# Kernel optimization log

Measured on AMD Instinct MI355X. Metric: run time of the kernel, lower is better.

Reference implementation:

```python
import jax, jax.numpy as jnp
import numpy as np

N, E, B = 100000, 1600000, 64
IN, HID, OUT, ED = 64, 128, 128, 2
K, ALPHA = 16, 0.1
LN_EPS = 1e-5


def setup_inputs() -> dict:
    key = jax.random.key(0)
    ks = jax.random.split(key, 24)
    def gl(k, shape, fan_in):
        return jax.random.uniform(k, shape, jnp.float32, -1.0, 1.0) / np.sqrt(fan_in)
    inp = {
        "x": jax.random.normal(ks[0], (N, IN), jnp.float32),
        "edge_index": jax.random.randint(ks[1], (2, E), 0, N, jnp.int64),
        "batch": jnp.sort(jax.random.randint(ks[2], (N,), 0, B, jnp.int64)),
        "edge_attr": jax.random.normal(ks[3], (E, ED), jnp.float32),
        # conv1: edge lin (ED->IN) + mlp (IN->HID->HID)
        "We1": gl(ks[4], (ED, IN), ED), "be1": jnp.zeros((IN,)),
        "W1a": gl(ks[5], (IN, HID), IN), "b1a": jnp.zeros((HID,)),
        "W1b": gl(ks[6], (HID, HID), HID), "b1b": jnp.zeros((HID,)),
        "g1": jnp.ones((HID,)), "bn1": jnp.zeros((HID,)),
        # conv2: edge lin (ED->HID) + mlp (HID->OUT->OUT)
        "We2": gl(ks[7], (ED, HID), ED), "be2": jnp.zeros((HID,)),
        "W2a": gl(ks[8], (HID, OUT), HID), "b2a": jnp.zeros((OUT,)),
        "W2b": gl(ks[9], (OUT, OUT), OUT), "b2b": jnp.zeros((OUT,)),
        "g2": jnp.ones((OUT,)), "bn2": jnp.zeros((OUT,)),
        # gate nn (OUT -> OUT//2 -> 1)
        "Wg1": gl(ks[10], (OUT, OUT // 2), OUT), "bg1": jnp.zeros((OUT // 2,)),
        "Wg2": gl(ks[11], (OUT // 2, 1), OUT // 2), "bg2": jnp.zeros((1,)),
    }
    return inp


def _gelu(x):
    return jax.nn.gelu(x, approximate=False)


def _layernorm(x, g, b):
    mu = jnp.mean(x, axis=-1, keepdims=True)
    var = jnp.mean(jnp.square(x - mu), axis=-1, keepdims=True)
    return (x - mu) * jax.lax.rsqrt(var + LN_EPS) * g + b


def _gine(x, src, dst, edge_attr, We, be, W1, b1, W2, b2):
    # message: ReLU(x_j + lin(edge_attr)), aggregated by sum at dst; eps=0
    m = jax.nn.relu(x[src] + edge_attr @ We + be)          # [E, d]
    agg = jax.ops.segment_sum(m, dst, num_segments=N)      # [N, d]
    h = x + agg
    return _gelu(h @ W1 + b1) @ W2 + b2


def _appnp(x, src, dst):
    # gcn_norm with self-loops: deg_i = 1 + in-degree
    deg = jax.ops.segment_sum(jnp.ones((E,), x.dtype), dst, num_segments=N) + 1.0
    dis = jax.lax.rsqrt(deg)
    w = dis[src] * dis[dst]            # [E]
    selfw = 1.0 / deg                  # [N]
    def step(i, h):
        prop = jax.ops.segment_sum(w[:, None] * h[src], dst, num_segments=N) \
               + selfw[:, None] * h
        return (1.0 - ALPHA) * prop + ALPHA * x
    return jax.lax.fori_loop(0, K, step, x)


def reference(x, edge_index, batch, edge_attr,
              We1, be1, W1a, b1a, W1b, b1b, g1, bn1,
              We2, be2, W2a, b2a, W2b, b2b, g2, bn2,
              Wg1, bg1, Wg2, bg2):
    src, dst = edge_index[0], edge_index[1]
    h = _gine(x, src, dst, edge_attr, We1, be1, W1a, b1a, W1b, b1b)
    h = _layernorm(_gelu(h), g1, bn1)
    # dropout is identity in eval
    h = _gine(h, src, dst, edge_attr, We2, be2, W2a, b2a, W2b, b2b)
    h = _layernorm(h, g2, bn2)
    h = _appnp(h, src, dst)
    # attentional aggregation: per-graph softmax over gate scores
    gate = (_gelu(h @ Wg1 + bg1) @ Wg2 + bg2)[:, 0]        # [N]
    m = jax.ops.segment_max(gate, batch, num_segments=B)    # [B]
    e = jnp.exp(gate - m[batch])
    s = jax.ops.segment_sum(e, batch, num_segments=B)
    a = e / s[batch]
    g = jax.ops.segment_sum(a[:, None] * h, batch, num_segments=B)  # [B, OUT]
    return h, g
```

## Files before the change

### kernel.cpp

```cpp
#include <hip/hip_runtime.h>
#include <math.h>

#define N_NODES 100000
#define N_EDGES 1600000
#define N_B 64
#define D_IN 64
#define D_HID 128
#define D_OUT 128
#define K_ITER 16
#define LN_EPS 1e-5f

typedef short s8v __attribute__((ext_vector_type(8)));
typedef float f4v __attribute__((ext_vector_type(4)));

__device__ __forceinline__ float gelu_f(float x) {
    return 0.5f * x * (1.0f + erff(0.70710678118654752440f * x));
}

__device__ __forceinline__ float ubx(unsigned u) { return __uint_as_float(u << 16); }
__device__ __forceinline__ float uby(unsigned u) { return __uint_as_float(u & 0xffff0000u); }

__device__ __forceinline__ unsigned short bf_rne(float x) {
    unsigned u = __float_as_uint(x);
    u += 0x7fffu + ((u >> 16) & 1u);
    return (unsigned short)(u >> 16);
}
__device__ __forceinline__ float bf_f(unsigned short s) {
    return __uint_as_float(((unsigned)s) << 16);
}
__device__ __forceinline__ unsigned pack_bf2(float a, float b) {
    return (unsigned)bf_rne(a) | (((unsigned)bf_rne(b)) << 16);
}


__global__ __launch_bounds__(256) void hist_kernel(const int* __restrict__ dst, int* __restrict__ counts) {
    int e = blockIdx.x * 256 + threadIdx.x;
    if (e < N_EDGES) atomicAdd(&counts[dst[e]], 1);
}

__global__ __launch_bounds__(256) void deg_kernel(const int* __restrict__ counts,
                                                  float* __restrict__ dis, float* __restrict__ selfw) {
    int i = blockIdx.x * 256 + threadIdx.x;
    if (i < N_NODES) {
        float d = (float)(counts[i] + 1);
        dis[i] = 1.0f / sqrtf(d);
        selfw[i] = 1.0f / d;
    }
}

__global__ __launch_bounds__(1024) void scan1(const int* __restrict__ counts, int* __restrict__ rp,
                                              int* __restrict__ bsum) {
    __shared__ int tmp[1024];
    int t = threadIdx.x;
    int idx = blockIdx.x * 1024 + t;
    int v = (idx < N_NODES) ? counts[idx] : 0;
    tmp[t] = v;
    __syncthreads();
    for (int o = 1; o < 1024; o <<= 1) {
        int add = (t >= o) ? tmp[t - o] : 0;
        __syncthreads();
        tmp[t] += add;
        __syncthreads();
    }
    if (idx < N_NODES) rp[idx] = tmp[t] - v;
    if (t == 1023) bsum[blockIdx.x] = tmp[t];
}

__global__ void scan2(int* bsum, int nb) {
    if (threadIdx.x == 0 && blockIdx.x == 0) {
        int acc = 0;
        for (int i = 0; i < nb; i++) { int v = bsum[i]; bsum[i] = acc; acc += v; }
    }
}

__global__ __launch_bounds__(1024) void scan3(int* __restrict__ rp, const int* __restrict__ bsum,
                                              int* __restrict__ cursor) {
    int t = threadIdx.x;
    int idx = blockIdx.x * 1024 + t;
    if (idx < N_NODES) {
        int v = rp[idx] + bsum[blockIdx.x];
        rp[idx] = v;
        cursor[idx] = v;
    }
    if (idx == 0) rp[N_NODES] = N_EDGES;
}

__global__ __launch_bounds__(256) void scatter_kernel(const int* __restrict__ src, const int* __restrict__ dst,
                                                      const float* __restrict__ ea,
                                                      int* __restrict__ cursor, int4* __restrict__ edata) {
    int e = blockIdx.x * 256 + threadIdx.x;
    if (e >= N_EDGES) return;
    int s = src[e], d = dst[e];
    int pos = atomicAdd(&cursor[d], 1);
    float2 e2 = ((const float2*)ea)[e];
    int4 v;
    v.x = s;
    v.y = __float_as_int(e2.x);
    v.z = __float_as_int(e2.y);
    v.w = 0;
    edata[pos] = v;
}

__global__ __launch_bounds__(256) void split_kernel(const int4* __restrict__ edata, int* __restrict__ esrc) {
    int e = blockIdx.x * 256 + threadIdx.x;
    if (e < N_EDGES) esrc[e] = edata[e].x;
}


__global__ __launch_bounds__(256) void conv1_gather(const float* __restrict__ x, const int* __restrict__ rp,
                                                    const int4* __restrict__ edata,
                                                    const float* __restrict__ We1, const float* __restrict__ be1,
                                                    float* __restrict__ out) {
    int gw = (blockIdx.x * 256 + threadIdx.x) >> 6;
    if (gw >= N_NODES) return;
    int lane = threadIdx.x & 63;
    float w0 = We1[lane], w1 = We1[64 + lane], bb = be1[lane];
    float acc = x[(size_t)gw * 64 + lane];
    int j = rp[gw], jend = rp[gw + 1];
    for (; j + 8 <= jend; j += 8) {
        int4 e0 = edata[j], e1 = edata[j + 1], e2 = edata[j + 2], e3 = edata[j + 3];
        int4 e4 = edata[j + 4], e5 = edata[j + 5], e6 = edata[j + 6], e7 = edata[j + 7];
        float v0 = x[(size_t)e0.x * 64 + lane];
        float v1 = x[(size_t)e1.x * 64 + lane];
        float v2 = x[(size_t)e2.x * 64 + lane];
        float v3 = x[(size_t)e3.x * 64 + lane];
        float v4 = x[(size_t)e4.x * 64 + lane];
        float v5 = x[(size_t)e5.x * 64 + lane];
        float v6 = x[(size_t)e6.x * 64 + lane];
        float v7 = x[(size_t)e7.x * 64 + lane];
        acc += fmaxf(v0 + __int_as_float(e0.y) * w0 + __int_as_float(e0.z) * w1 + bb, 0.0f);
        acc += fmaxf(v1 + __int_as_float(e1.y) * w0 + __int_as_float(e1.z) * w1 + bb, 0.0f);
        acc += fmaxf(v2 + __int_as_float(e2.y) * w0 + __int_as_float(e2.z) * w1 + bb, 0.0f);
        acc += fmaxf(v3 + __int_as_float(e3.y) * w0 + __int_as_float(e3.z) * w1 + bb, 0.0f);
        acc += fmaxf(v4 + __int_as_float(e4.y) * w0 + __int_as_float(e4.z) * w1 + bb, 0.0f);
        acc += fmaxf(v5 + __int_as_float(e5.y) * w0 + __int_as_float(e5.z) * w1 + bb, 0.0f);
        acc += fmaxf(v6 + __int_as_float(e6.y) * w0 + __int_as_float(e6.z) * w1 + bb, 0.0f);
        acc += fmaxf(v7 + __int_as_float(e7.y) * w0 + __int_as_float(e7.z) * w1 + bb, 0.0f);
    }
    for (; j < jend; j++) {
        int4 e = edata[j];
        float v = x[(size_t)e.x * 64 + lane];
        acc += fmaxf(v + __int_as_float(e.y) * w0 + __int_as_float(e.z) * w1 + bb, 0.0f);
    }
    out[(size_t)gw * 64 + lane] = acc;
}

__global__ __launch_bounds__(256) void conv2_gather(const float* __restrict__ h1f, const unsigned* __restrict__ h1b,
                                                    const int* __restrict__ rp,
                                                    const int4* __restrict__ edata,
                                                    const float* __restrict__ We2, const float* __restrict__ be2,
                                                    float* __restrict__ out) {
    int gw = (blockIdx.x * 256 + threadIdx.x) >> 6;
    if (gw >= N_NODES) return;
    int lane = threadIdx.x & 63;
    int f0 = lane * 2;
    float w00 = We2[f0], w01 = We2[f0 + 1];
    float w10 = We2[128 + f0], w11 = We2[128 + f0 + 1];
    float b0 = be2[f0], b1 = be2[f0 + 1];
    float2 hc = ((const float2*)h1f)[(size_t)gw * 64 + lane];
    float a0 = hc.x, a1 = hc.y;
    int j = rp[gw], jend = rp[gw + 1];
    for (; j + 8 <= jend; j += 8) {
        int4 e0 = edata[j], e1 = edata[j + 1], e2 = edata[j + 2], e3 = edata[j + 3];
        int4 e4 = edata[j + 4], e5 = edata[j + 5], e6 = edata[j + 6], e7 = edata[j + 7];
        unsigned v0 = h1b[(size_t)e0.x * 64 + lane];
        unsigned v1 = h1b[(size_t)e1.x * 64 + lane];
        unsigned v2 = h1b[(size_t)e2.x * 64 + lane];
        unsigned v3 = h1b[(size_t)e3.x * 64 + lane];
        unsigned v4 = h1b[(size_t)e4.x * 64 + lane];
        unsigned v5 = h1b[(size_t)e5.x * 64 + lane];
        unsigned v6 = h1b[(size_t)e6.x * 64 + lane];
        unsigned v7 = h1b[(size_t)e7.x * 64 + lane];
        a0 += fmaxf(ubx(v0) + __int_as_float(e0.y) * w00 + __int_as_float(e0.z) * w10 + b0, 0.0f);
        a1 += fmaxf(uby(v0) + __int_as_float(e0.y) * w01 + __int_as_float(e0.z) * w11 + b1, 0.0f);
        a0 += fmaxf(ubx(v1) + __int_as_float(e1.y) * w00 + __int_as_float(e1.z) * w10 + b0, 0.0f);
        a1 += fmaxf(uby(v1) + __int_as_float(e1.y) * w01 + __int_as_float(e1.z) * w11 + b1, 0.0f);
        a0 += fmaxf(ubx(v2) + __int_as_float(e2.y) * w00 + __int_as_float(e2.z) * w10 + b0, 0.0f);
        a1 += fmaxf(uby(v2) + __int_as_float(e2.y) * w01 + __int_as_float(e2.z) * w11 + b1, 0.0f);
        a0 += fmaxf(ubx(v3) + __int_as_float(e3.y) * w00 + __int_as_float(e3.z) * w10 + b0, 0.0f);
        a1 += fmaxf(uby(v3) + __int_as_float(e3.y) * w01 + __int_as_float(e3.z) * w11 + b1, 0.0f);
        a0 += fmaxf(ubx(v4) + __int_as_float(e4.y) * w00 + __int_as_float(e4.z) * w10 + b0, 0.0f);
        a1 += fmaxf(uby(v4) + __int_as_float(e4.y) * w01 + __int_as_float(e4.z) * w11 + b1, 0.0f);
        a0 += fmaxf(ubx(v5) + __int_as_float(e5.y) * w00 + __int_as_float(e5.z) * w10 + b0, 0.0f);
        a1 += fmaxf(uby(v5) + __int_as_float(e5.y) * w01 + __int_as_float(e5.z) * w11 + b1, 0.0f);
        a0 += fmaxf(ubx(v6) + __int_as_float(e6.y) * w00 + __int_as_float(e6.z) * w10 + b0, 0.0f);
        a1 += fmaxf(uby(v6) + __int_as_float(e6.y) * w01 + __int_as_float(e6.z) * w11 + b1, 0.0f);
        a0 += fmaxf(ubx(v7) + __int_as_float(e7.y) * w00 + __int_as_float(e7.z) * w10 + b0, 0.0f);
        a1 += fmaxf(uby(v7) + __int_as_float(e7.y) * w01 + __int_as_float(e7.z) * w11 + b1, 0.0f);
    }
    for (; j < jend; j++) {
        int4 e = edata[j];
        unsigned v = h1b[(size_t)e.x * 64 + lane];
        a0 += fmaxf(ubx(v) + __int_as_float(e.y) * w00 + __int_as_float(e.z) * w10 + b0, 0.0f);
        a1 += fmaxf(uby(v) + __int_as_float(e.y) * w01 + __int_as_float(e.z) * w11 + b1, 0.0f);
    }
    out[(size_t)gw * 128 + f0] = a0;
    out[(size_t)gw * 128 + f0 + 1] = a1;
}


template <int Kd, bool GELU, bool LN, int OMODE>
__global__ __launch_bounds__(256) void mlp_mfma(const float* __restrict__ A, const float* __restrict__ W,
                                                const float* __restrict__ bias, const float* __restrict__ g,
                                                const float* __restrict__ bn, float* __restrict__ outf,
                                                unsigned short* __restrict__ outb) {
    __shared__ unsigned short sHi[8192];
    __shared__ unsigned short sLo[8192];
    int wave = threadIdx.x >> 6, lane = threadIdx.x & 63;
    int quad = lane >> 4, n = lane & 15;
    int rowA = blockIdx.x * 64 + wave * 16 + n;
    int rowAc = (rowA < N_NODES) ? rowA : 0;

    f4v acc[8];
    #pragma unroll
    for (int t = 0; t < 8; t++) acc[t] = (f4v){0.f, 0.f, 0.f, 0.f};

    for (int ph = 0; ph < Kd / 64; ph++) {
        __syncthreads();
        for (int idx = threadIdx.x; idx < 8192; idx += 256) {
            int k = idx >> 7, c = idx & 127;
            float v = W[(size_t)(ph * 64 + k) * 128 + c];
            unsigned short hi = bf_rne(v);
            unsigned short lo = bf_rne(v - bf_f(hi));
            int kk = k >> 5, q = (k >> 3) & 3, j = k & 7, t = c >> 4, nn = c & 15;
            int lidx = ((((kk * 4 + q) * 8 + t) * 16 + nn) << 3) + j;
            sHi[lidx] = hi;
            sLo[lidx] = lo;
        }
        __syncthreads();
        #pragma unroll
        for (int kk = 0; kk < 2; kk++) {
            int k0 = ph * 64 + kk * 32 + quad * 8;
            const float4* ap = (const float4*)(A + (size_t)rowAc * Kd + k0);
            float4 a0 = ap[0], a1 = ap[1];
            float av[8] = {a0.x, a0.y, a0.z, a0.w, a1.x, a1.y, a1.z, a1.w};
            s8v ahi, alo;
            #pragma unroll
            for (int j = 0; j < 8; j++) {
                unsigned short h = bf_rne(av[j]);
                ahi[j] = (short)h;
                alo[j] = (short)bf_rne(av[j] - bf_f(h));
            }
            int base = ((kk * 4 + quad) * 8) * 128;
            #pragma unroll
            for (int t = 0; t < 8; t++) {
                s8v bhi = *(const s8v*)&sHi[base + ((t * 16 + n) << 3)];
                s8v blo = *(const s8v*)&sLo[base + ((t * 16 + n) << 3)];
                acc[t] = __builtin_amdgcn_mfma_f32_16x16x32_bf16(ahi, bhi, acc[t], 0, 0, 0);
                acc[t] = __builtin_amdgcn_mfma_f32_16x16x32_bf16(ahi, blo, acc[t], 0, 0, 0);
                acc[t] = __builtin_amdgcn_mfma_f32_16x16x32_bf16(alo, bhi, acc[t], 0, 0, 0);
            }
        }
    }

    float bcol[8], gcol[8], bncol[8];
    #pragma unroll
    for (int t = 0; t < 8; t++) {
        bcol[t] = bias[t * 16 + n];
        if (LN) { gcol[t] = g[t * 16 + n]; bncol[t] = bn[t * 16 + n]; }
    }
    #pragma unroll
    for (int r = 0; r < 4; r++) {
        int row = blockIdx.x * 64 + wave * 16 + quad * 4 + r;
        float v[8];
        #pragma unroll
        for (int t = 0; t < 8; t++) {
            float x = acc[t][r] + bcol[t];
            v[t] = GELU ? gelu_f(x) : x;
        }
        if (LN) {
            float s = 0.f, q2 = 0.f;
            #pragma unroll
            for (int t = 0; t < 8; t++) { s += v[t]; q2 += v[t] * v[t]; }
            #pragma unroll
            for (int m = 1; m <= 8; m <<= 1) {
                s += __shfl_xor(s, m, 64);
                q2 += __shfl_xor(q2, m, 64);
            }
            float mu = s * (1.0f / 128.0f);
            float rs = rsqrtf(q2 * (1.0f / 128.0f) - mu * mu + LN_EPS);
            #pragma unroll
            for (int t = 0; t < 8; t++) v[t] = (v[t] - mu) * rs * gcol[t] + bncol[t];
        }
        if (row < N_NODES) {
            #pragma unroll
            for (int t = 0; t < 8; t++) {
                if (OMODE != 2) outf[(size_t)row * 128 + t * 16 + n] = v[t];
                if (OMODE >= 1) outb[(size_t)row * 128 + t * 16 + n] = bf_rne(v[t]);
            }
        }
    }
}


__global__ __launch_bounds__(256) void gate_mfma(const float* __restrict__ h, const float* __restrict__ Wg1,
                                                 const float* __restrict__ bg1, const float* __restrict__ Wg2,
                                                 const float* __restrict__ bg2, float* __restrict__ gate) {
    __shared__ unsigned short sHi[8192];
    __shared__ unsigned short sLo[8192];
    int wave = threadIdx.x >> 6, lane = threadIdx.x & 63;
    int quad = lane >> 4, n = lane & 15;
    for (int idx = threadIdx.x; idx < 8192; idx += 256) {
        int k = idx >> 6, c = idx & 63;
        float v = Wg1[k * 64 + c];
        unsigned short hi = bf_rne(v);
        unsigned short lo = bf_rne(v - bf_f(hi));
        int kk = k >> 5, q = (k >> 3) & 3, j = k & 7, t = c >> 4, nn = c & 15;
        int lidx = ((((kk * 4 + q) * 4 + t) * 16 + nn) << 3) + j;
        sHi[lidx] = hi;
        sLo[lidx] = lo;
    }
    __syncthreads();
    int rowA = blockIdx.x * 64 + wave * 16 + n;
    int rowAc = (rowA < N_NODES) ? rowA : 0;
    f4v acc[4];
    #pragma unroll
    for (int t = 0; t < 4; t++) acc[t] = (f4v){0.f, 0.f, 0.f, 0.f};
    #pragma unroll
    for (int kk = 0; kk < 4; kk++) {
        const float4* ap = (const float4*)(h + (size_t)rowAc * 128 + kk * 32 + quad * 8);
        float4 a0 = ap[0], a1 = ap[1];
        float av[8] = {a0.x, a0.y, a0.z, a0.w, a1.x, a1.y, a1.z, a1.w};
        s8v ahi, alo;
        #pragma unroll
        for (int j = 0; j < 8; j++) {
            unsigned short hh = bf_rne(av[j]);
            ahi[j] = (short)hh;
            alo[j] = (short)bf_rne(av[j] - bf_f(hh));
        }
        int base = ((kk * 4 + quad) * 4) * 128;
        #pragma unroll
        for (int t = 0; t < 4; t++) {
            s8v bhi = *(const s8v*)&sHi[base + ((t * 16 + n) << 3)];
            s8v blo = *(const s8v*)&sLo[base + ((t * 16 + n) << 3)];
            acc[t] = __builtin_amdgcn_mfma_f32_16x16x32_bf16(ahi, bhi, acc[t], 0, 0, 0);
            acc[t] = __builtin_amdgcn_mfma_f32_16x16x32_bf16(ahi, blo, acc[t], 0, 0, 0);
            acc[t] = __builtin_amdgcn_mfma_f32_16x16x32_bf16(alo, bhi, acc[t], 0, 0, 0);
        }
    }
    float b2 = bg2[0];
    float bb[4], vv[4];
    #pragma unroll
    for (int t = 0; t < 4; t++) { bb[t] = bg1[t * 16 + n]; vv[t] = Wg2[t * 16 + n]; }
    #pragma unroll
    for (int r = 0; r < 4; r++) {
        int row = blockIdx.x * 64 + wave * 16 + quad * 4 + r;
        float val = 0.f;
        #pragma unroll
        for (int t = 0; t < 4; t++) val += gelu_f(acc[t][r] + bb[t]) * vv[t];
        #pragma unroll
        for (int m = 1; m <= 8; m <<= 1) val += __shfl_xor(val, m, 64);
        if (n == 0 && row < N_NODES) gate[row] = val + b2;
    }
}


template <bool LAST>
__global__ __launch_bounds__(256) void appnp_step_bf(const unsigned* __restrict__ hin,
                                                     const unsigned* __restrict__ anchor,
                                                     unsigned* __restrict__ hout, float2* __restrict__ houtf,
                                                     const int* __restrict__ rp, const int* __restrict__ esrc,
                                                     const float* __restrict__ dis,
                                                     const float* __restrict__ selfw) {
    int gw = (blockIdx.x * 256 + threadIdx.x) >> 6;
    if (gw >= N_NODES) return;
    int lane = threadIdx.x & 63;
    size_t idx = (size_t)gw * 64 + lane;
    float swi = selfw[gw];
    float wd = dis[gw];
    unsigned hcp = hin[idx];
    float ax = swi * ubx(hcp), ay = swi * uby(hcp);
    int j = rp[gw], jend = rp[gw + 1];
    for (; j + 8 <= jend; j += 8) {
        int s0 = esrc[j],     s1 = esrc[j + 1], s2 = esrc[j + 2], s3 = esrc[j + 3];
        int s4 = esrc[j + 4], s5 = esrc[j + 5], s6 = esrc[j + 6], s7 = esrc[j + 7];
        unsigned v0 = hin[(size_t)s0 * 64 + lane];
        unsigned v1 = hin[(size_t)s1 * 64 + lane];
        unsigned v2 = hin[(size_t)s2 * 64 + lane];
        unsigned v3 = hin[(size_t)s3 * 64 + lane];
        unsigned v4 = hin[(size_t)s4 * 64 + lane];
        unsigned v5 = hin[(size_t)s5 * 64 + lane];
        unsigned v6 = hin[(size_t)s6 * 64 + lane];
        unsigned v7 = hin[(size_t)s7 * 64 + lane];
        float w0 = dis[s0] * wd, w1 = dis[s1] * wd, w2 = dis[s2] * wd, w3 = dis[s3] * wd;
        float w4 = dis[s4] * wd, w5 = dis[s5] * wd, w6 = dis[s6] * wd, w7 = dis[s7] * wd;
        ax = fmaf(w0, ubx(v0), ax); ay = fmaf(w0, uby(v0), ay);
        ax = fmaf(w1, ubx(v1), ax); ay = fmaf(w1, uby(v1), ay);
        ax = fmaf(w2, ubx(v2), ax); ay = fmaf(w2, uby(v2), ay);
        ax = fmaf(w3, ubx(v3), ax); ay = fmaf(w3, uby(v3), ay);
        ax = fmaf(w4, ubx(v4), ax); ay = fmaf(w4, uby(v4), ay);
        ax = fmaf(w5, ubx(v5), ax); ay = fmaf(w5, uby(v5), ay);
        ax = fmaf(w6, ubx(v6), ax); ay = fmaf(w6, uby(v6), ay);
        ax = fmaf(w7, ubx(v7), ax); ay = fmaf(w7, uby(v7), ay);
    }
    for (; j + 4 <= jend; j += 4) {
        int s0 = esrc[j], s1 = esrc[j + 1], s2 = esrc[j + 2], s3 = esrc[j + 3];
        unsigned v0 = hin[(size_t)s0 * 64 + lane];
        unsigned v1 = hin[(size_t)s1 * 64 + lane];
        unsigned v2 = hin[(size_t)s2 * 64 + lane];
        unsigned v3 = hin[(size_t)s3 * 64 + lane];
        float w0 = dis[s0] * wd, w1 = dis[s1] * wd, w2 = dis[s2] * wd, w3 = dis[s3] * wd;
        ax = fmaf(w0, ubx(v0), ax); ay = fmaf(w0, uby(v0), ay);
        ax = fmaf(w1, ubx(v1), ax); ay = fmaf(w1, uby(v1), ay);
        ax = fmaf(w2, ubx(v2), ax); ay = fmaf(w2, uby(v2), ay);
        ax = fmaf(w3, ubx(v3), ax); ay = fmaf(w3, uby(v3), ay);
    }
    for (; j < jend; j++) {
        int s = esrc[j];
        unsigned v = hin[(size_t)s * 64 + lane];
        float w = dis[s] * wd;
        ax = fmaf(w, ubx(v), ax); ay = fmaf(w, uby(v), ay);
    }
    unsigned ancp = anchor[idx];
    float ox = 0.9f * ax + 0.1f * ubx(ancp);
    float oy = 0.9f * ay + 0.1f * uby(ancp);
    if (LAST) {
        float2 o; o.x = ox; o.y = oy;
        houtf[idx] = o;
    } else {
        hout[idx] = pack_bf2(ox, oy);
    }
}


__global__ void seg_begin(const int* __restrict__ batch, int* __restrict__ gbeg) {
    int b = threadIdx.x;
    if (b > N_B) return;
    if (b == N_B) { gbeg[N_B] = N_NODES; return; }
    int lo = 0, hi = N_NODES;
    while (lo < hi) {
        int mid = (lo + hi) >> 1;
        if (batch[mid] < b) lo = mid + 1; else hi = mid;
    }
    gbeg[b] = lo;
}

__global__ __launch_bounds__(256) void seg_max(const float* __restrict__ gate, const int* __restrict__ gbeg,
                                               float* __restrict__ gmax) {
    int b = blockIdx.x;
    int s = gbeg[b], e = gbeg[b + 1];
    float m = -INFINITY;
    for (int i = s + threadIdx.x; i < e; i += 256) m = fmaxf(m, gate[i]);
    for (int o = 32; o > 0; o >>= 1) m = fmaxf(m, __shfl_xor(m, o, 64));
    __shared__ float red[4];
    if ((threadIdx.x & 63) == 0) red[threadIdx.x >> 6] = m;
    __syncthreads();
    if (threadIdx.x == 0) gmax[b] = fmaxf(fmaxf(red[0], red[1]), fmaxf(red[2], red[3]));
}

__global__ __launch_bounds__(256) void seg_sum(const float* __restrict__ gate, const int* __restrict__ gbeg,
                                               const float* __restrict__ gmax, float* __restrict__ gsum) {
    int b = blockIdx.x;
    int s = gbeg[b], e = gbeg[b + 1];
    float m = gmax[b];
    float acc = 0.0f;
    for (int i = s + threadIdx.x; i < e; i += 256) acc += expf(gate[i] - m);
    for (int o = 32; o > 0; o >>= 1) acc += __shfl_xor(acc, o, 64);
    __shared__ float red[4];
    if ((threadIdx.x & 63) == 0) red[threadIdx.x >> 6] = acc;
    __syncthreads();
    if (threadIdx.x == 0) gsum[b] = red[0] + red[1] + red[2] + red[3];
}

__global__ __launch_bounds__(512) void seg_pool(const float* __restrict__ h, const float* __restrict__ gate,
                                                const int* __restrict__ gbeg, const float* __restrict__ gmax,
                                                const float* __restrict__ gsum, float* __restrict__ gout) {
    int b = blockIdx.x >> 3, slice = blockIdx.x & 7;
    int team = threadIdx.x >> 7;
    int f = threadIdx.x & 127;
    int s = gbeg[b], e = gbeg[b + 1];
    float m = gmax[b];
    float inv = (e > s) ? 1.0f / gsum[b] : 0.0f;
    float acc = 0.0f;
    for (int i = s + slice * 4 + team; i < e; i += 32) {
        float a = expf(gate[i] - m) * inv;
        acc = fmaf(a, h[(size_t)i * 128 + f], acc);
    }
    __shared__ float red[4][128];
    red[team][f] = acc;
    __syncthreads();
    if (team == 0) {
        float v = red[0][f] + red[1][f] + red[2][f] + red[3][f];
        atomicAdd(&gout[b * 128 + f], v);
    }
}


extern "C" void kernel_launch(void* const* d_in, const int* in_sizes, int n_in,
                              void* d_out, int out_size, void* d_ws, size_t ws_size,
                              hipStream_t stream) {
    const float* x     = (const float*)d_in[0];
    const int*   ei    = (const int*)d_in[1];
    const int*   batch = (const int*)d_in[2];
    const float* ea    = (const float*)d_in[3];
    const float* We1 = (const float*)d_in[4];
    const float* be1 = (const float*)d_in[5];
    const float* W1a = (const float*)d_in[6];
    const float* b1a = (const float*)d_in[7];
    const float* W1b = (const float*)d_in[8];
    const float* b1b = (const float*)d_in[9];
    const float* g1  = (const float*)d_in[10];
    const float* bn1 = (const float*)d_in[11];
    const float* We2 = (const float*)d_in[12];
    const float* be2 = (const float*)d_in[13];
    const float* W2a = (const float*)d_in[14];
    const float* b2a = (const float*)d_in[15];
    const float* W2b = (const float*)d_in[16];
    const float* b2b = (const float*)d_in[17];
    const float* g2  = (const float*)d_in[18];
    const float* bn2 = (const float*)d_in[19];
    const float* Wg1 = (const float*)d_in[20];
    const float* bg1 = (const float*)d_in[21];
    const float* Wg2 = (const float*)d_in[22];
    const float* bg2 = (const float*)d_in[23];

    float* outH = (float*)d_out;
    float* outG = outH + (size_t)N_NODES * 128;

    char* w = (char*)d_ws;
    auto carve = [&](size_t bytes) {
        void* p = (void*)w;
        w += ((bytes + 255) / 256) * 256;
        return p;
    };
    float*  bufB   = (float*)carve((size_t)N_NODES * 128 * 4);
    float*  bufC   = (float*)carve((size_t)N_NODES * 128 * 4);
    int4*   edata  = (int4*)carve((size_t)N_EDGES * 16);
    int*    counts = (int*)carve((size_t)N_NODES * 4);
    int*    rp     = (int*)carve((size_t)(N_NODES + 1) * 4);
    int*    cursor = (int*)carve((size_t)N_NODES * 4);
    float*  dis    = (float*)carve((size_t)N_NODES * 4);
    float*  selfw  = (float*)carve((size_t)N_NODES * 4);
    float*  gate   = (float*)carve((size_t)N_NODES * 4);
    int*    bsum   = (int*)carve(128 * 4);
    float*  gmax   = (float*)carve(N_B * 4);
    float*  gsum   = (float*)carve(N_B * 4);
    int*    gbeg   = (int*)carve((N_B + 1) * 4);

    const int* src = ei;
    const int* dst = ei + N_EDGES;

    const int NB_SCAN = (N_NODES + 1023) / 1024;
    const int EB = (N_EDGES + 255) / 256;
    const int NBLK = (N_NODES + 255) / 256;
    const int WBLK = (N_NODES + 3) / 4;
    const int MBLK = (N_NODES + 63) / 64;

    hipMemsetAsync(counts, 0, (size_t)N_NODES * 4, stream);
    hist_kernel<<<EB, 256, 0, stream>>>(dst, counts);
    deg_kernel<<<NBLK, 256, 0, stream>>>(counts, dis, selfw);
    scan1<<<NB_SCAN, 1024, 0, stream>>>(counts, rp, bsum);
    scan2<<<1, 64, 0, stream>>>(bsum, NB_SCAN);
    scan3<<<NB_SCAN, 1024, 0, stream>>>(rp, bsum, cursor);
    scatter_kernel<<<EB, 256, 0, stream>>>(src, dst, ea, cursor, edata);

    unsigned short* h1bf  = (unsigned short*)bufC;
    unsigned* ancU  = (unsigned*)bufC;
    unsigned* pingA = ancU + (size_t)N_NODES * 64;
    unsigned* pingB = (unsigned*)bufB;
    int*      esrc  = (int*)(bufB + (size_t)N_NODES * 64);

    conv1_gather<<<WBLK, 256, 0, stream>>>(x, rp, edata, We1, be1, bufB);
    mlp_mfma<64, true, false, 0><<<MBLK, 256, 0, stream>>>(bufB, W1a, b1a, nullptr, nullptr, outH, nullptr);
    mlp_mfma<128, true, true, 1><<<MBLK, 256, 0, stream>>>(outH, W1b, b1b, g1, bn1, bufB, h1bf);

    conv2_gather<<<WBLK, 256, 0, stream>>>(bufB, (const unsigned*)h1bf, rp, edata, We2, be2, outH);
    mlp_mfma<128, true, false, 0><<<MBLK, 256, 0, stream>>>(outH, W2a, b2a, nullptr, nullptr, bufB, nullptr);
    mlp_mfma<128, false, true, 2><<<MBLK, 256, 0, stream>>>(bufB, W2b, b2b, g2, bn2, nullptr, (unsigned short*)ancU);

    split_kernel<<<EB, 256, 0, stream>>>(edata, esrc);

    const unsigned* cur = ancU;
    for (int k = 1; k <= K_ITER - 1; k++) {
        unsigned* dstbuf = (k & 1) ? pingA : pingB;
        appnp_step_bf<false><<<WBLK, 256, 0, stream>>>(cur, ancU, dstbuf, nullptr, rp, esrc, dis, selfw);
        cur = dstbuf;
    }
    appnp_step_bf<true><<<WBLK, 256, 0, stream>>>(cur, ancU, nullptr, (float2*)outH, rp, esrc, dis, selfw);

    gate_mfma<<<MBLK, 256, 0, stream>>>(outH, Wg1, bg1, Wg2, bg2, gate);
    seg_begin<<<1, 128, 0, stream>>>(batch, gbeg);
    seg_max<<<N_B, 256, 0, stream>>>(gate, gbeg, gmax);
    seg_sum<<<N_B, 256, 0, stream>>>(gate, gbeg, gmax, gsum);
    hipMemsetAsync(outG, 0, (size_t)N_B * 128 * 4, stream);
    seg_pool<<<N_B * 8, 512, 0, stream>>>(outH, gate, gbeg, gmax, gsum, outG);
}
```

Measured before the change: 1.860 ms.

## Rescale APPNP state by D^-1/2 to drop per-edge weights; gather conv1 x in bf16

The APPNP iteration now works on u = D^-1/2 h, so each edge contribution is a plain sum and the per-edge dis[src] loads and multiplies are removed. The self-loop and final scale use 0.9*selfw and sqrt(deg). The anchor is pre-scaled by dis when written from the last MLP, and the final step rescales by sqrt(deg) to recover h. Separately, x is converted to bf16 so the conv1 neighbor gather reads half the bytes, at the cost of an extra conversion kernel and reduced precision in the conv1 messages.

New measurement: 1.779 ms. 1.05x faster.

```diff
diff --git a/kernel.cpp b/kernel.cpp
--- a/kernel.cpp
+++ b/kernel.cpp
@@ -39,12 +39,14 @@
 }
 
 __global__ __launch_bounds__(256) void deg_kernel(const int* __restrict__ counts,
-                                                  float* __restrict__ dis, float* __restrict__ selfw) {
+                                                  float* __restrict__ dis, float* __restrict__ selfw,
+                                                  float* __restrict__ rsq) {
     int i = blockIdx.x * 256 + threadIdx.x;
     if (i < N_NODES) {
         float d = (float)(counts[i] + 1);
         dis[i] = 1.0f / sqrtf(d);
         selfw[i] = 1.0f / d;
+        rsq[i] = sqrtf(d);
     }
 }
 
@@ -106,8 +108,21 @@
     if (e < N_EDGES) esrc[e] = edata[e].x;
 }
 
-
-__global__ __launch_bounds__(256) void conv1_gather(const float* __restrict__ x, const int* __restrict__ rp,
+__global__ __launch_bounds__(256) void x_to_bf(const float4* __restrict__ x4, uint2* __restrict__ xb2) {
+    int i = blockIdx.x * 256 + threadIdx.x;
+    if (i < N_NODES * 16) {
+        float4 v = x4[i];
+        uint2 o;
+        o.x = pack_bf2(v.x, v.y);
+        o.y = pack_bf2(v.z, v.w);
+        xb2[i] = o;
+    }
+}
+
+
+__global__ __launch_bounds__(256) void conv1_gather(const float* __restrict__ x,
+                                                    const unsigned short* __restrict__ xb,
+                                                    const int* __restrict__ rp,
                                                     const int4* __restrict__ edata,
                                                     const float* __restrict__ We1, const float* __restrict__ be1,
                                                     float* __restrict__ out) {
@@ -120,27 +135,27 @@
     for (; j + 8 <= jend; j += 8) {
         int4 e0 = edata[j], e1 = edata[j + 1], e2 = edata[j + 2], e3 = edata[j + 3];
         int4 e4 = edata[j + 4], e5 = edata[j + 5], e6 = edata[j + 6], e7 = edata[j + 7];
-        float v0 = x[(size_t)e0.x * 64 + lane];
-        float v1 = x[(size_t)e1.x * 64 + lane];
-        float v2 = x[(size_t)e2.x * 64 + lane];
-        float v3 = x[(size_t)e3.x * 64 + lane];
-        float v4 = x[(size_t)e4.x * 64 + lane];
-        float v5 = x[(size_t)e5.x * 64 + lane];
-        float v6 = x[(size_t)e6.x * 64 + lane];
-        float v7 = x[(size_t)e7.x * 64 + lane];
-        acc += fmaxf(v0 + __int_as_float(e0.y) * w0 + __int_as_float(e0.z) * w1 + bb, 0.0f);
-        acc += fmaxf(v1 + __int_as_float(e1.y) * w0 + __int_as_float(e1.z) * w1 + bb, 0.0f);
-        acc += fmaxf(v2 + __int_as_float(e2.y) * w0 + __int_as_float(e2.z) * w1 + bb, 0.0f);
-        acc += fmaxf(v3 + __int_as_float(e3.y) * w0 + __int_as_float(e3.z) * w1 + bb, 0.0f);
-        acc += fmaxf(v4 + __int_as_float(e4.y) * w0 + __int_as_float(e4.z) * w1 + bb, 0.0f);
-        acc += fmaxf(v5 + __int_as_float(e5.y) * w0 + __int_as_float(e5.z) * w1 + bb, 0.0f);
-        acc += fmaxf(v6 + __int_as_float(e6.y) * w0 + __int_as_float(e6.z) * w1 + bb, 0.0f);
-        acc += fmaxf(v7 + __int_as_float(e7.y) * w0 + __int_as_float(e7.z) * w1 + bb, 0.0f);
+        unsigned short v0 = xb[(size_t)e0.x * 64 + lane];
+        unsigned short v1 = xb[(size_t)e1.x * 64 + lane];
+        unsigned short v2 = xb[(size_t)e2.x * 64 + lane];
+        unsigned short v3 = xb[(size_t)e3.x * 64 + lane];
+        unsigned short v4 = xb[(size_t)e4.x * 64 + lane];
+        unsigned short v5 = xb[(size_t)e5.x * 64 + lane];
+        unsigned short v6 = xb[(size_t)e6.x * 64 + lane];
+        unsigned short v7 = xb[(size_t)e7.x * 64 + lane];
+        acc += fmaxf(bf_f(v0) + __int_as_float(e0.y) * w0 + __int_as_float(e0.z) * w1 + bb, 0.0f);
+        acc += fmaxf(bf_f(v1) + __int_as_float(e1.y) * w0 + __int_as_float(e1.z) * w1 + bb, 0.0f);
+        acc += fmaxf(bf_f(v2) + __int_as_float(e2.y) * w0 + __int_as_float(e2.z) * w1 + bb, 0.0f);
+        acc += fmaxf(bf_f(v3) + __int_as_float(e3.y) * w0 + __int_as_float(e3.z) * w1 + bb, 0.0f);
+        acc += fmaxf(bf_f(v4) + __int_as_float(e4.y) * w0 + __int_as_float(e4.z) * w1 + bb, 0.0f);
+        acc += fmaxf(bf_f(v5) + __int_as_float(e5.y) * w0 + __int_as_float(e5.z) * w1 + bb, 0.0f);
+        acc += fmaxf(bf_f(v6) + __int_as_float(e6.y) * w0 + __int_as_float(e6.z) * w1 + bb, 0.0f);
+        acc += fmaxf(bf_f(v7) + __int_as_float(e7.y) * w0 + __int_as_float(e7.z) * w1 + bb, 0.0f);
     }
     for (; j < jend; j++) {
         int4 e = edata[j];
-        float v = x[(size_t)e.x * 64 + lane];
-        acc += fmaxf(v + __int_as_float(e.y) * w0 + __int_as_float(e.z) * w1 + bb, 0.0f);
+        unsigned short v = xb[(size_t)e.x * 64 + lane];
+        acc += fmaxf(bf_f(v) + __int_as_float(e.y) * w0 + __int_as_float(e.z) * w1 + bb, 0.0f);
     }
     out[(size_t)gw * 64 + lane] = acc;
 }
@@ -199,11 +214,12 @@
 }
 
 
-template <int Kd, bool GELU, bool LN, int OMODE>
+template <int Kd, bool GELU, bool LN, int OMODE, bool SCALE>
 __global__ __launch_bounds__(256) void mlp_mfma(const float* __restrict__ A, const float* __restrict__ W,
                                                 const float* __restrict__ bias, const float* __restrict__ g,
                                                 const float* __restrict__ bn, float* __restrict__ outf,
-                                                unsigned short* __restrict__ outb) {
+                                                unsigned short* __restrict__ outb,
+                                                const float* __restrict__ uscale) {
     __shared__ unsigned short sHi[8192];
     __shared__ unsigned short sLo[8192];
     int wave = threadIdx.x >> 6, lane = threadIdx.x & 63;
@@ -283,10 +299,11 @@
             for (int t = 0; t < 8; t++) v[t] = (v[t] - mu) * rs * gcol[t] + bncol[t];
         }
         if (row < N_NODES) {
+            float us = SCALE ? uscale[row] : 1.0f;
             #pragma unroll
             for (int t = 0; t < 8; t++) {
                 if (OMODE != 2) outf[(size_t)row * 128 + t * 16 + n] = v[t];
-                if (OMODE >= 1) outb[(size_t)row * 128 + t * 16 + n] = bf_rne(v[t]);
+                if (OMODE >= 1) outb[(size_t)row * 128 + t * 16 + n] = bf_rne(SCALE ? v[t] * us : v[t]);
             }
         }
     }
@@ -356,20 +373,18 @@
 
 
 template <bool LAST>
-__global__ __launch_bounds__(256) void appnp_step_bf(const unsigned* __restrict__ hin,
-                                                     const unsigned* __restrict__ anchor,
-                                                     unsigned* __restrict__ hout, float2* __restrict__ houtf,
-                                                     const int* __restrict__ rp, const int* __restrict__ esrc,
-                                                     const float* __restrict__ dis,
-                                                     const float* __restrict__ selfw) {
+__global__ __launch_bounds__(256) void appnp_step_u(const unsigned* __restrict__ hin,
+                                                    const unsigned* __restrict__ anchor,
+                                                    unsigned* __restrict__ hout, float2* __restrict__ houtf,
+                                                    const int* __restrict__ rp, const int* __restrict__ esrc,
+                                                    const float* __restrict__ selfw,
+                                                    const float* __restrict__ rsq) {
     int gw = (blockIdx.x * 256 + threadIdx.x) >> 6;
     if (gw >= N_NODES) return;
     int lane = threadIdx.x & 63;
     size_t idx = (size_t)gw * 64 + lane;
-    float swi = selfw[gw];
-    float wd = dis[gw];
     unsigned hcp = hin[idx];
-    float ax = swi * ubx(hcp), ay = swi * uby(hcp);
+    float ax = ubx(hcp), ay = uby(hcp);
     int j = rp[gw], jend = rp[gw + 1];
     for (; j + 8 <= jend; j += 8) {
         int s0 = esrc[j],     s1 = esrc[j + 1], s2 = esrc[j + 2], s3 = esrc[j + 3];
@@ -382,16 +397,14 @@
         unsigned v5 = hin[(size_t)s5 * 64 + lane];
         unsigned v6 = hin[(size_t)s6 * 64 + lane];
         unsigned v7 = hin[(size_t)s7 * 64 + lane];
-        float w0 = dis[s0] * wd, w1 = dis[s1] * wd, w2 = dis[s2] * wd, w3 = dis[s3] * wd;
-        float w4 = dis[s4] * wd, w5 = dis[s5] * wd, w6 = dis[s6] * wd, w7 = dis[s7] * wd;
-        ax = fmaf(w0, ubx(v0), ax); ay = fmaf(w0, uby(v0), ay);
-        ax = fmaf(w1, ubx(v1), ax); ay = fmaf(w1, uby(v1), ay);
-        ax = fmaf(w2, ubx(v2), ax); ay = fmaf(w2, uby(v2), ay);
-        ax = fmaf(w3, ubx(v3), ax); ay = fmaf(w3, uby(v3), ay);
-        ax = fmaf(w4, ubx(v4), ax); ay = fmaf(w4, uby(v4), ay);
-        ax = fmaf(w5, ubx(v5), ax); ay = fmaf(w5, uby(v5), ay);
-        ax = fmaf(w6, ubx(v6), ax); ay = fmaf(w6, uby(v6), ay);
-        ax = fmaf(w7, ubx(v7), ax); ay = fmaf(w7, uby(v7), ay);
+        ax += ubx(v0); ay += uby(v0);
+        ax += ubx(v1); ay += uby(v1);
+        ax += ubx(v2); ay += uby(v2);
+        ax += ubx(v3); ay += uby(v3);
+        ax += ubx(v4); ay += uby(v4);
+        ax += ubx(v5); ay += uby(v5);
+        ax += ubx(v6); ay += uby(v6);
+        ax += ubx(v7); ay += uby(v7);
     }
     for (; j + 4 <= jend; j += 4) {
         int s0 = esrc[j], s1 = esrc[j + 1], s2 = esrc[j + 2], s3 = esrc[j + 3];
@@ -399,23 +412,23 @@
         unsigned v1 = hin[(size_t)s1 * 64 + lane];
         unsigned v2 = hin[(size_t)s2 * 64 + lane];
         unsigned v3 = hin[(size_t)s3 * 64 + lane];
-        float w0 = dis[s0] * wd, w1 = dis[s1] * wd, w2 = dis[s2] * wd, w3 = dis[s3] * wd;
-        ax = fmaf(w0, ubx(v0), ax); ay = fmaf(w0, uby(v0), ay);
-        ax = fmaf(w1, ubx(v1), ax); ay = fmaf(w1, uby(v1), ay);
-        ax = fmaf(w2, ubx(v2), ax); ay = fmaf(w2, uby(v2), ay);
-        ax = fmaf(w3, ubx(v3), ax); ay = fmaf(w3, uby(v3), ay);
+        ax += ubx(v0); ay += uby(v0);
+        ax += ubx(v1); ay += uby(v1);
+        ax += ubx(v2); ay += uby(v2);
+        ax += ubx(v3); ay += uby(v3);
     }
     for (; j < jend; j++) {
         int s = esrc[j];
         unsigned v = hin[(size_t)s * 64 + lane];
-        float w = dis[s] * wd;
-        ax = fmaf(w, ubx(v), ax); ay = fmaf(w, uby(v), ay);
-    }
+        ax += ubx(v); ay += uby(v);
+    }
+    float swi = 0.9f * selfw[gw];
     unsigned ancp = anchor[idx];
-    float ox = 0.9f * ax + 0.1f * ubx(ancp);
-    float oy = 0.9f * ay + 0.1f * uby(ancp);
+    float ox = fmaf(swi, ax, 0.1f * ubx(ancp));
+    float oy = fmaf(swi, ay, 0.1f * uby(ancp));
     if (LAST) {
-        float2 o; o.x = ox; o.y = oy;
+        float rq = rsq[gw];
+        float2 o; o.x = ox * rq; o.y = oy * rq;
         houtf[idx] = o;
     } else {
         hout[idx] = pack_bf2(ox, oy);
@@ -531,6 +544,7 @@
     int*    cursor = (int*)carve((size_t)N_NODES * 4);
     float*  dis    = (float*)carve((size_t)N_NODES * 4);
     float*  selfw  = (float*)carve((size_t)N_NODES * 4);
+    float*  rsq    = (float*)carve((size_t)N_NODES * 4);
     float*  gate   = (float*)carve((size_t)N_NODES * 4);
     int*    bsum   = (int*)carve(128 * 4);
     float*  gmax   = (float*)carve(N_B * 4);
@@ -546,37 +560,39 @@
     const int WBLK = (N_NODES + 3) / 4;
     const int MBLK = (N_NODES + 63) / 64;
 
+    unsigned short* h1bf  = (unsigned short*)bufC;
+    unsigned* ancU  = (unsigned*)bufC;
+    unsigned* pingA = ancU + (size_t)N_NODES * 64;
+    unsigned* pingB = (unsigned*)bufB;
+    unsigned short* xb = (unsigned short*)pingA;
+    int*      esrc  = (int*)(bufB + (size_t)N_NODES * 64);
+
     hipMemsetAsync(counts, 0, (size_t)N_NODES * 4, stream);
     hist_kernel<<<EB, 256, 0, stream>>>(dst, counts);
-    deg_kernel<<<NBLK, 256, 0, stream>>>(counts, dis, selfw);
+    deg_kernel<<<NBLK, 256, 0, stream>>>(counts, dis, selfw, rsq);
     scan1<<<NB_SCAN, 1024, 0, stream>>>(counts, rp, bsum);
     scan2<<<1, 64, 0, stream>>>(bsum, NB_SCAN);
     scan3<<<NB_SCAN, 1024, 0, stream>>>(rp, bsum, cursor);
     scatter_kernel<<<EB, 256, 0, stream>>>(src, dst, ea, cursor, edata);
-
-    unsigned short* h1bf  = (unsigned short*)bufC;
-    unsigned* ancU  = (unsigned*)bufC;
-    unsigned* pingA = ancU + (size_t)N_NODES * 64;
-    unsigned* pingB = (unsigned*)bufB;
-    int*      esrc  = (int*)(bufB + (size_t)N_NODES * 64);
-
-    conv1_gather<<<WBLK, 256, 0, stream>>>(x, rp, edata, We1, be1, bufB);
-    mlp_mfma<64, true, false, 0><<<MBLK, 256, 0, stream>>>(bufB, W1a, b1a, nullptr, nullptr, outH, nullptr);
-    mlp_mfma<128, true, true, 1><<<MBLK, 256, 0, stream>>>(outH, W1b, b1b, g1, bn1, bufB, h1bf);
+    x_to_bf<<<(N_NODES * 16 + 255) / 256, 256, 0, stream>>>((const float4*)x, (uint2*)xb);
+
+    conv1_gather<<<WBLK, 256, 0, stream>>>(x, xb, rp, edata, We1, be1, bufB);
+    mlp_mfma<64, true, false, 0, false><<<MBLK, 256, 0, stream>>>(bufB, W1a, b1a, nullptr, nullptr, outH, nullptr, nullptr);
+    mlp_mfma<128, true, true, 1, false><<<MBLK, 256, 0, stream>>>(outH, W1b, b1b, g1, bn1, bufB, h1bf, nullptr);
 
     conv2_gather<<<WBLK, 256, 0, stream>>>(bufB, (const unsigned*)h1bf, rp, edata, We2, be2, outH);
-    mlp_mfma<128, true, false, 0><<<MBLK, 256, 0, stream>>>(outH, W2a, b2a, nullptr, nullptr, bufB, nullptr);
-    mlp_mfma<128, false, true, 2><<<MBLK, 256, 0, stream>>>(bufB, W2b, b2b, g2, bn2, nullptr, (unsigned short*)ancU);
+    mlp_mfma<128, true, false, 0, false><<<MBLK, 256, 0, stream>>>(outH, W2a, b2a, nullptr, nullptr, bufB, nullptr, nullptr);
+    mlp_mfma<128, false, true, 2, true><<<MBLK, 256, 0, stream>>>(bufB, W2b, b2b, g2, bn2, nullptr, (unsigned short*)ancU, dis);
 
     split_kernel<<<EB, 256, 0, stream>>>(edata, esrc);
 
     const unsigned* cur = ancU;
     for (int k = 1; k <= K_ITER - 1; k++) {
         unsigned* dstbuf = (k & 1) ? pingA : pingB;
-        appnp_step_bf<false><<<WBLK, 256, 0, stream>>>(cur, ancU, dstbuf, nullptr, rp, esrc, dis, selfw);
+        appnp_step_u<false><<<WBLK, 256, 0, stream>>>(cur, ancU, dstbuf, nullptr, rp, esrc, selfw, nullptr);
         cur = dstbuf;
     }
-    appnp_step_bf<true><<<WBLK, 256, 0, stream>>>(cur, ancU, nullptr, (float2*)outH, rp, esrc, dis, selfw);
+    appnp_step_u<true><<<WBLK, 256, 0, stream>>>(cur, ancU, nullptr, (float2*)outH, rp, esrc, selfw, rsq);
 
     gate_mfma<<<MBLK, 256, 0, stream>>>(outH, Wg1, bg1, Wg2, bg2, gate);
     seg_begin<<<1, 128, 0, stream>>>(batch, gbeg);
```
